# Performance work log

Measured on AMD Instinct MI355X. Metric: run time of the kernel, lower is better.

Reference implementation:

```python
import jax, jax.numpy as jnp
import numpy as np

NEG = -1e9  # finite stand-in for -inf (avoids inf-inf NaNs, safe in fp32)


def setup_inputs() -> dict:
    T, V, Lmax, A = 2048, 8192, 8, 64
    rng = np.random.default_rng(0)
    seq = rng.integers(0, A, size=T).astype(np.int32)
    # first A pieces are the single codepoints -> every sequence is segmentable
    piece_lens = np.concatenate([
        np.ones(A, np.int32),
        rng.integers(1, Lmax + 1, size=V - A).astype(np.int32),
    ])
    pieces = rng.integers(0, A, size=(V, Lmax)).astype(np.int32)
    pieces[:A, 0] = np.arange(A)
    logits = rng.standard_normal(V).astype(np.float32)
    m = logits.max()
    log_probs = (logits - m - np.log(np.exp(logits - m).sum())).astype(np.float32)
    return {
        'seq': jnp.asarray(seq),
        'pieces': jnp.asarray(pieces),
        'piece_lens': jnp.asarray(piece_lens),
        'log_probs': jnp.asarray(log_probs),
    }


def reference(seq, pieces, piece_lens, log_probs):
    T = seq.shape[0]
    V, Lmax = pieces.shape
    dt = log_probs.dtype

    # --- match table: match[t, i] = piece i matches sequence at position t ---
    seq_pad = jnp.concatenate([seq, jnp.full((Lmax,), -1, seq.dtype)])
    windows = seq_pad[jnp.arange(T)[:, None] + jnp.arange(Lmax)[None, :]]  # [T, Lmax]
    lmask = jnp.arange(Lmax)[None, :] < piece_lens[:, None]                # [V, Lmax]
    eq = windows[:, None, :] == pieces[None, :, :]                        # [T, V, Lmax]
    fits = (jnp.arange(T)[:, None] + piece_lens[None, :]) <= T            # [T, V]
    match = jnp.all(eq | ~lmask[None, :, :], axis=-1) & fits              # [T, V]
    mlp = jnp.where(match, log_probs[None, :], NEG).astype(dt)            # [T, V]

    # end_logp[t-1, i] = mlp[t - len_i, i]  (piece i ending exactly at t, t=1..T)
    te = jnp.arange(1, T + 1)[:, None]
    src = te - piece_lens[None, :]
    end_logp = jnp.where(src >= 0,
                         mlp[jnp.clip(src, 0, T - 1), jnp.arange(V)[None, :]],
                         NEG)

    # --- forward pass: alpha[t] = logsumexp_i alpha[t - len_i] + log p_i ---
    idx_a = Lmax - piece_lens  # window slot holding alpha[t - len_i]
    def fstep(win, row):
        a_t = jax.nn.logsumexp(win[idx_a] + row)
        return jnp.concatenate([win[1:], a_t[None]]), a_t
    win0 = jnp.full((Lmax,), NEG, dt).at[-1].set(0.0)
    _, alpha_rest = jax.lax.scan(fstep, win0, end_logp)
    alpha = jnp.concatenate([jnp.zeros((1,), dt), alpha_rest])  # [T+1]

    # --- backward pass: beta[t] = logsumexp_i log p_i + beta[t + len_i] ---
    idx_b = piece_lens - 1  # window slot holding beta[t + len_i]
    def bstep(win, row):
        b_t = jax.nn.logsumexp(row + win[idx_b])
        return jnp.concatenate([b_t[None], win[:-1]]), b_t
    winT = jnp.full((Lmax,), NEG, dt).at[0].set(0.0)
    _, beta_rev = jax.lax.scan(bstep, winT, mlp[::-1])
    beta = jnp.concatenate([beta_rev[::-1], jnp.zeros((1,), dt)])  # [T+1]

    # --- posteriors: P[t, i] = exp(alpha[t] + log p_i + beta[t+len_i] - alpha[T]) ---
    norm = alpha[T]
    beta_next = beta[jnp.clip(jnp.arange(T)[:, None] + piece_lens[None, :], 0, T)]
    P = jnp.exp(alpha[:T][:, None] + mlp + beta_next - norm)
    P = jnp.where(match, P, 0.0)
    return jnp.where(norm > NEG / 2, P, jnp.zeros_like(P))
```

## Files before the change

kernel.cpp:

```cpp
#include <hip/hip_runtime.h>
#include <stdint.h>

#define LMAX 8
#define KCH 32
#define NC  64
#define LN2D 0.6931471805599453

struct __align__(16) PK { unsigned long long key; float logp; int len; };

__device__ __forceinline__ int exp2i(double m) {
  return (int)((__double_as_longlong(m) >> 52) & 0x7ff) - 1023;
}
__device__ __forceinline__ double pow2d(int e) {
  return __longlong_as_double((long long)(1023 + e) << 52);
}

__global__ void k_prep(const int* __restrict__ seq, const int* __restrict__ pieces,
                       const int* __restrict__ plens, const float* __restrict__ logp,
                       PK* __restrict__ pk, unsigned long long* __restrict__ w64,
                       float* __restrict__ M, int T, int V) {
  int idx = blockIdx.x * blockDim.x + threadIdx.x;
  if (idx < V) {
    const int* pr = pieces + idx * LMAX;
    int len = plens[idx];
    unsigned long long key = 0ull;
    #pragma unroll
    for (int l = 0; l < LMAX; ++l) {
      unsigned long long b = (unsigned long long)(pr[l] & 0xFF);
      if (l < len) key |= b << (8 * l);
    }
    PK o; o.key = key; o.logp = logp[idx]; o.len = len;
    pk[idx] = o;
  } else if (idx < V + T) {
    int t = idx - V;
    unsigned long long w = 0ull;
    #pragma unroll
    for (int l = 0; l < LMAX; ++l) {
      int pos = t + l;
      unsigned long long b = (pos < T) ? (unsigned long long)(seq[pos] & 0xFF) : 0xFFull;
      w |= b << (8 * l);
    }
    w64[t] = w;
  } else if (idx < V + T + T * LMAX) {
    M[idx - V - T] = 0.f;
  }
}

__global__ void k_match(const PK* __restrict__ pk, const unsigned long long* __restrict__ w64,
                        float* __restrict__ M, int T, int V, int tPer) {
  int v = blockIdx.x * blockDim.x + threadIdx.x;
  PK p = pk[v];
  unsigned long long mask = (p.len >= 8) ? ~0ull : ((1ull << (8 * p.len)) - 1ull);
  unsigned long long key = p.key;
  int t0 = blockIdx.y * tPer;
  float prob = -1.f;
  for (int t = t0; t < t0 + tPer; ++t) {
    unsigned long long w = w64[t];
    if (((w ^ key) & mask) == 0ull) {
      if (prob < 0.f) prob = expf(p.logp);
      atomicAdd(&M[t * LMAX + (p.len - 1)], prob);
    }
  }
}

__global__ __launch_bounds__(256) void k_scan(const float* __restrict__ M,
        double* __restrict__ aD, double* __restrict__ bD,
        float* __restrict__ aL, float* __restrict__ bL, int T) {
  __shared__ float  Wt[2][64][65];
  __shared__ double Ust[2][NC][8];
  __shared__ int    EW[2][NC];
  __shared__ int    Eacc[2][NC];
  const int tid = threadIdx.x;
  const float4* Mv = (const float4*)M;

  {
    const int dir = tid >> 7;
    const int lt  = tid & 127;
    const int c   = lt >> 1, h = lt & 1;
    const int base = c * KCH;
    double st[8][4];
    #pragma unroll
    for (int i = 0; i < 8; ++i)
      #pragma unroll
      for (int bb = 0; bb < 4; ++bb)
        st[i][bb] = (i == 4 * h + bb) ? 1.0 : 0.0;

    if (dir == 0) {
      float4 ra = Mv[base * 2], rb = Mv[base * 2 + 1];
      for (int kg = 0; kg < KCH / 8; ++kg) {
        #pragma unroll
        for (int kk = 0; kk < 8; ++kk) {
          int k = kg * 8 + kk;
          float4 c0 = ra, c1 = rb;
          int nk = (k + 1 < KCH) ? k + 1 : KCH - 1;
          ra = Mv[(base + nk) * 2]; rb = Mv[(base + nk) * 2 + 1];
          double r0=c0.x,r1=c0.y,r2=c0.z,r3=c0.w,r4=c1.x,r5=c1.y,r6=c1.z,r7=c1.w;
          #pragma unroll
          for (int bb = 0; bb < 4; ++bb) {
            double a_ = st[kk & 7][bb];
            st[(kk+1)&7][bb] = fma(a_, r0, st[(kk+1)&7][bb]);
            st[(kk+2)&7][bb] = fma(a_, r1, st[(kk+2)&7][bb]);
            st[(kk+3)&7][bb] = fma(a_, r2, st[(kk+3)&7][bb]);
            st[(kk+4)&7][bb] = fma(a_, r3, st[(kk+4)&7][bb]);
            st[(kk+5)&7][bb] = fma(a_, r4, st[(kk+5)&7][bb]);
            st[(kk+6)&7][bb] = fma(a_, r5, st[(kk+6)&7][bb]);
            st[(kk+7)&7][bb] = fma(a_, r6, st[(kk+7)&7][bb]);
            st[kk & 7][bb]   = a_ * r7;
          }
        }
      }
    } else {
      float4 ra = Mv[(base + KCH - 1) * 2], rb = Mv[(base + KCH - 1) * 2 + 1];
      for (int kg = 0; kg < KCH / 8; ++kg) {
        #pragma unroll
        for (int kk = 0; kk < 8; ++kk) {
          int k = kg * 8 + kk;
          float4 c0 = ra, c1 = rb;
          int nk = (k + 1 < KCH) ? k + 1 : KCH - 1;
          int nt = base + KCH - 1 - nk;
          ra = Mv[nt * 2]; rb = Mv[nt * 2 + 1];
          double r0=c0.x,r1=c0.y,r2=c0.z,r3=c0.w,r4=c1.x,r5=c1.y,r6=c1.z,r7=c1.w;
          #pragma unroll
          for (int bb = 0; bb < 4; ++bb) {
            double nb =            r0 * st[(8 -kk)&7][bb];
            nb = fma(r1, st[(9 -kk)&7][bb], nb);
            nb = fma(r2, st[(10-kk)&7][bb], nb);
            nb = fma(r3, st[(11-kk)&7][bb], nb);
            nb = fma(r4, st[(12-kk)&7][bb], nb);
            nb = fma(r5, st[(13-kk)&7][bb], nb);
            nb = fma(r6, st[(14-kk)&7][bb], nb);
            nb = fma(r7, st[(15-kk)&7][bb], nb);
            st[(7 - kk) & 7][bb] = nb;
          }
        }
      }
    }
    double mx = 0.0;
    #pragma unroll
    for (int i = 0; i < 8; ++i)
      #pragma unroll
      for (int bb = 0; bb < 4; ++bb) mx = fmax(mx, st[i][bb]);
    mx = fmax(mx, __shfl_xor(mx, 1));
    int e = exp2i(mx);
    double sc = pow2d(-e);
    #pragma unroll
    for (int i = 0; i < 8; ++i)
      #pragma unroll
      for (int bb = 0; bb < 4; ++bb)
        Wt[dir][i * 8 + 4 * h + bb][c] = (float)(st[i][bb] * sc);
    if (h == 0) EW[dir][c] = e;
  }
  __syncthreads();

  {
    int wv = tid >> 6;
    if ((wv & 1) == 0) {
      const int dir = wv >> 1;
      const int l = tid & 63;
      double uj = ((l & 7) == 0) ? 1.0 : 0.0;
      int ea = 0;
      int c0 = dir ? (NC - 1) : 0;
      double wcur = (double)Wt[dir][l][c0];
      for (int ci = 0; ci < NC; ++ci) {
        int c = dir ? (NC - 1 - ci) : ci;
        int cn = dir ? (NC - 2 - ci) : (ci + 1);
        if (l < 8) Ust[dir][c][l] = uj;
        if (l == 0) Eacc[dir][c] = ea;
        double wnext = (ci + 1 < NC) ? (double)Wt[dir][l][cn] : 0.0;
        double p = wcur * uj;
        p += __shfl_xor(p, 1);
        p += __shfl_xor(p, 2);
        p += __shfl_xor(p, 4);
        uj = __shfl(p, ((l & 7) << 3) | (l >> 3));
        ea += EW[dir][c];
        if (ci & 1) {
          double m = uj;
          m = fmax(m, __shfl_xor(m, 1));
          m = fmax(m, __shfl_xor(m, 2));
          m = fmax(m, __shfl_xor(m, 4));
          int ex = exp2i(m);
          uj *= pow2d(-ex);
          ea += ex;
        }
        wcur = wnext;
      }
    }
  }
  __syncthreads();

  {
    int wv = tid >> 6;
    int c = tid & 63;
    int base = c * KCH;
    if (wv == 0) {
      double st[8];
      #pragma unroll
      for (int i = 0; i < 8; ++i) st[i] = Ust[0][c][i];
      float4 ra = Mv[base * 2], rb = Mv[base * 2 + 1];
      for (int kg = 0; kg < KCH / 8; ++kg) {
        #pragma unroll
        for (int kk = 0; kk < 8; ++kk) {
          int k = kg * 8 + kk;
          float4 c0 = ra, c1 = rb;
          int nk = (k + 1 < KCH) ? k + 1 : KCH - 1;
          ra = Mv[(base + nk) * 2]; rb = Mv[(base + nk) * 2 + 1];
          double r0=c0.x,r1=c0.y,r2=c0.z,r3=c0.w,r4=c1.x,r5=c1.y,r6=c1.z,r7=c1.w;
          double a_ = st[kk & 7];
          st[(kk+1)&7] = fma(a_, r0, st[(kk+1)&7]);
          st[(kk+2)&7] = fma(a_, r1, st[(kk+2)&7]);
          st[(kk+3)&7] = fma(a_, r2, st[(kk+3)&7]);
          st[(kk+4)&7] = fma(a_, r3, st[(kk+4)&7]);
          st[(kk+5)&7] = fma(a_, r4, st[(kk+5)&7]);
          st[(kk+6)&7] = fma(a_, r5, st[(kk+6)&7]);
          st[(kk+7)&7] = fma(a_, r6, st[(kk+7)&7]);
          st[kk & 7]   = a_ * r7;
          aD[base + k + 1] = st[(kk + 1) & 7];
        }
      }
    } else if (wv == 2) {
      double st[8];
      #pragma unroll
      for (int i = 0; i < 8; ++i) st[i] = Ust[1][c][i];
      float4 ra = Mv[(base + KCH - 1) * 2], rb = Mv[(base + KCH - 1) * 2 + 1];
      for (int kg = 0; kg < KCH / 8; ++kg) {
        #pragma unroll
        for (int kk = 0; kk < 8; ++kk) {
          int k = kg * 8 + kk;
          int t = base + KCH - 1 - k;
          float4 c0 = ra, c1 = rb;
          int nk = (k + 1 < KCH) ? k + 1 : KCH - 1;
          int nt = base + KCH - 1 - nk;
          ra = Mv[nt * 2]; rb = Mv[nt * 2 + 1];
          double r0=c0.x,r1=c0.y,r2=c0.z,r3=c0.w,r4=c1.x,r5=c1.y,r6=c1.z,r7=c1.w;
          double nb =            r0 * st[(8 -kk)&7];
          nb = fma(r1, st[(9 -kk)&7], nb);
          nb = fma(r2, st[(10-kk)&7], nb);
          nb = fma(r3, st[(11-kk)&7], nb);
          nb = fma(r4, st[(12-kk)&7], nb);
          nb = fma(r5, st[(13-kk)&7], nb);
          nb = fma(r6, st[(14-kk)&7], nb);
          nb = fma(r7, st[(15-kk)&7], nb);
          st[(7 - kk) & 7] = nb;
          bD[t] = nb;
        }
      }
    }
  }
  __syncthreads();

  for (int t = tid; t <= T; t += 256) {
    float av = 0.f, bv = 0.f;
    if (t > 0)  av = (float)(log(aD[t]) + (double)Eacc[0][(t - 1) >> 5] * LN2D);
    if (t < T)  bv = (float)(log(bD[t]) + (double)Eacc[1][t >> 5] * LN2D);
    aL[t] = av; bL[t] = bv;
  }
}

__global__ void k_out(const PK* __restrict__ pk, const unsigned long long* __restrict__ w64,
                      const float* __restrict__ aL, const float* __restrict__ bL,
                      float* __restrict__ out, int T, int V, int tPer) {
  int v = blockIdx.x * blockDim.x + threadIdx.x;
  PK p = pk[v];
  unsigned long long mask = (p.len >= 8) ? ~0ull : ((1ull << (8 * p.len)) - 1ull);
  unsigned long long key = p.key;
  float norm = aL[T];
  float base = p.logp - norm;
  int t0 = blockIdx.y * tPer;
  for (int t = t0; t < t0 + tPer; ++t) {
    unsigned long long w = w64[t];
    float val = 0.f;
    if (((w ^ key) & mask) == 0ull)
      val = __expf(aL[t] + base + bL[t + p.len]);
    out[(size_t)t * V + v] = val;
  }
}

extern "C" void kernel_launch(void* const* d_in, const int* in_sizes, int n_in,
                              void* d_out, int out_size, void* d_ws, size_t ws_size,
                              hipStream_t stream) {
  const int* seq    = (const int*)d_in[0];
  const int* pieces = (const int*)d_in[1];
  const int* plens  = (const int*)d_in[2];
  const float* logp = (const float*)d_in[3];
  float* out = (float*)d_out;
  const int T = in_sizes[0];
  const int V = in_sizes[2];

  char* p = (char*)d_ws;
  PK* pk = (PK*)p;                     p += (size_t)V * sizeof(PK);
  unsigned long long* w64 = (unsigned long long*)p; p += (size_t)T * 8;
  float* M = (float*)p;                p += (size_t)T * LMAX * 4;
  double* aD = (double*)p;             p += (size_t)(T + 1) * 8;
  double* bD = (double*)p;             p += (size_t)(T + 1) * 8;
  float* aL = (float*)p;               p += (size_t)(T + 1) * 4;
  float* bL = (float*)p;               p += (size_t)(T + 1) * 4;

  int prepN = V + T + T * LMAX;
  k_prep<<<(prepN + 255) / 256, 256, 0, stream>>>(seq, pieces, plens, logp, pk, w64, M, T, V);

  const int tPer2 = 128;
  dim3 g2(V / 256, T / tPer2);
  k_match<<<g2, 256, 0, stream>>>(pk, w64, M, T, V, tPer2);

  k_scan<<<1, 256, 0, stream>>>(M, aD, bD, aL, bL, T);

  const int tPer5 = 32;
  dim3 g5(V / 256, T / tPer5);
  k_out<<<g5, 256, 0, stream>>>(pk, w64, aL, bL, out, T, V, tPer5);
}
```

Measured before the change: 72.51 us.

## Replace serial chunk-carry scan with two-level parallel transfer-matrix scan in fp32

The single-block scan kernel now builds per-chunk 8x8 transfer matrices in fp32 with periodic power-of-two renormalisation, using 512 threads. The sequential 64-step carry propagation becomes a two-level scheme: eight groups compose eight chunks each, then a short serial scan over group products produces per-chunk prefix states. The log step also splits doubles into exponent and mantissa so it can use log2f instead of a double-precision log. The goal is to shorten the latency-bound serial chain in this one-block kernel, at the cost of more exponent bookkeeping, global scratch buffers for intermediate matrices, and extra synchronisation phases.

```diff
diff --git a/kernel.cpp b/kernel.cpp
--- a/kernel.cpp
+++ b/kernel.cpp
@@ -4,16 +4,16 @@
 #define LMAX 8
 #define KCH 32
 #define NC  64
+#define TT  2048
 #define LN2D 0.6931471805599453
+#define NEGE (-(1<<28))
 
 struct __align__(16) PK { unsigned long long key; float logp; int len; };
 
-__device__ __forceinline__ int exp2i(double m) {
-  return (int)((__double_as_longlong(m) >> 52) & 0x7ff) - 1023;
-}
-__device__ __forceinline__ double pow2d(int e) {
-  return __longlong_as_double((long long)(1023 + e) << 52);
-}
+__device__ __forceinline__ int fexp(float m) { return ((__float_as_int(m) >> 23) & 0xFF) - 127; }
+__device__ __forceinline__ int fexpbits(float m) { return (__float_as_int(m) >> 23) & 0xFF; }
+__device__ __forceinline__ float p2(int e) { return __int_as_float((e + 127) << 23); }
+__device__ __forceinline__ float p2c(int e) { return (e < -126) ? 0.f : p2(e); }
 
 __global__ void k_prep(const int* __restrict__ seq, const int* __restrict__ pieces,
                        const int* __restrict__ plens, const float* __restrict__ logp,
@@ -63,55 +63,73 @@
   }
 }
 
-__global__ __launch_bounds__(256) void k_scan(const float* __restrict__ M,
+__global__ __launch_bounds__(512) void k_scan(const float* __restrict__ M,
+        float* __restrict__ Wt, float* __restrict__ P,
         double* __restrict__ aD, double* __restrict__ bD,
-        float* __restrict__ aL, float* __restrict__ bL, int T) {
-  __shared__ float  Wt[2][64][65];
-  __shared__ double Ust[2][NC][8];
-  __shared__ int    EW[2][NC];
-  __shared__ int    Eacc[2][NC];
+        float* __restrict__ aL, float* __restrict__ bL) {
+  __shared__ float  Gm[2 * 8 * 69];
+  __shared__ float  Cs[2 * 64 * 9];
+  __shared__ float  Sg[2 * 8 * 9];
+  __shared__ int    EWc[2 * 64 * 8];
+  __shared__ int    EPs[2 * 64 * 8];
+  __shared__ int    EGs[2 * 8 * 8];
+  __shared__ int    EaccP[2 * 64];
+  __shared__ int    EsB[2 * 8];
   const int tid = threadIdx.x;
   const float4* Mv = (const float4*)M;
 
   {
-    const int dir = tid >> 7;
-    const int lt  = tid & 127;
-    const int c   = lt >> 1, h = lt & 1;
+    const int dir = tid >> 8, lt = tid & 255;
+    const int c = lt >> 2, h = lt & 3;
     const int base = c * KCH;
-    double st[8][4];
-    #pragma unroll
-    for (int i = 0; i < 8; ++i)
-      #pragma unroll
-      for (int bb = 0; bb < 4; ++bb)
-        st[i][bb] = (i == 4 * h + bb) ? 1.0 : 0.0;
-
+    float st[2][8];
+    #pragma unroll
+    for (int bb = 0; bb < 2; ++bb)
+      #pragma unroll
+      for (int i = 0; i < 8; ++i) st[bb][i] = (i == 2 * h + bb) ? p2(64) : 0.f;
+    int ec = -64;
     if (dir == 0) {
       float4 ra = Mv[base * 2], rb = Mv[base * 2 + 1];
-      for (int kg = 0; kg < KCH / 8; ++kg) {
+      for (int kg = 0; kg < 4; ++kg) {
         #pragma unroll
         for (int kk = 0; kk < 8; ++kk) {
           int k = kg * 8 + kk;
           float4 c0 = ra, c1 = rb;
           int nk = (k + 1 < KCH) ? k + 1 : KCH - 1;
           ra = Mv[(base + nk) * 2]; rb = Mv[(base + nk) * 2 + 1];
-          double r0=c0.x,r1=c0.y,r2=c0.z,r3=c0.w,r4=c1.x,r5=c1.y,r6=c1.z,r7=c1.w;
           #pragma unroll
-          for (int bb = 0; bb < 4; ++bb) {
-            double a_ = st[kk & 7][bb];
-            st[(kk+1)&7][bb] = fma(a_, r0, st[(kk+1)&7][bb]);
-            st[(kk+2)&7][bb] = fma(a_, r1, st[(kk+2)&7][bb]);
-            st[(kk+3)&7][bb] = fma(a_, r2, st[(kk+3)&7][bb]);
-            st[(kk+4)&7][bb] = fma(a_, r3, st[(kk+4)&7][bb]);
-            st[(kk+5)&7][bb] = fma(a_, r4, st[(kk+5)&7][bb]);
-            st[(kk+6)&7][bb] = fma(a_, r5, st[(kk+6)&7][bb]);
-            st[(kk+7)&7][bb] = fma(a_, r6, st[(kk+7)&7][bb]);
-            st[kk & 7][bb]   = a_ * r7;
+          for (int bb = 0; bb < 2; ++bb) {
+            float a_ = st[bb][kk & 7];
+            st[bb][(kk + 1) & 7] = fmaf(a_, c0.x, st[bb][(kk + 1) & 7]);
+            st[bb][(kk + 2) & 7] = fmaf(a_, c0.y, st[bb][(kk + 2) & 7]);
+            st[bb][(kk + 3) & 7] = fmaf(a_, c0.z, st[bb][(kk + 3) & 7]);
+            st[bb][(kk + 4) & 7] = fmaf(a_, c0.w, st[bb][(kk + 4) & 7]);
+            st[bb][(kk + 5) & 7] = fmaf(a_, c1.x, st[bb][(kk + 5) & 7]);
+            st[bb][(kk + 6) & 7] = fmaf(a_, c1.y, st[bb][(kk + 6) & 7]);
+            st[bb][(kk + 7) & 7] = fmaf(a_, c1.z, st[bb][(kk + 7) & 7]);
+            st[bb][kk & 7]       = a_ * c1.w;
+          }
+          if (kk == 3 || kk == 7) {
+            float mx = 0.f;
+            #pragma unroll
+            for (int bb = 0; bb < 2; ++bb)
+              #pragma unroll
+              for (int i = 0; i < 8; ++i) mx = fmaxf(mx, st[bb][i]);
+            if (fexpbits(mx) != 0) {
+              int e = fexp(mx), d = 64 - e;
+              float m1 = p2(d / 2), m2 = p2(d - d / 2);
+              #pragma unroll
+              for (int bb = 0; bb < 2; ++bb)
+                #pragma unroll
+                for (int i = 0; i < 8; ++i) st[bb][i] = st[bb][i] * m1 * m2;
+              ec += e - 64;
+            }
           }
         }
       }
     } else {
       float4 ra = Mv[(base + KCH - 1) * 2], rb = Mv[(base + KCH - 1) * 2 + 1];
-      for (int kg = 0; kg < KCH / 8; ++kg) {
+      for (int kg = 0; kg < 4; ++kg) {
         #pragma unroll
         for (int kk = 0; kk < 8; ++kk) {
           int k = kg * 8 + kk;
@@ -119,139 +137,275 @@
           int nk = (k + 1 < KCH) ? k + 1 : KCH - 1;
           int nt = base + KCH - 1 - nk;
           ra = Mv[nt * 2]; rb = Mv[nt * 2 + 1];
-          double r0=c0.x,r1=c0.y,r2=c0.z,r3=c0.w,r4=c1.x,r5=c1.y,r6=c1.z,r7=c1.w;
           #pragma unroll
-          for (int bb = 0; bb < 4; ++bb) {
-            double nb =            r0 * st[(8 -kk)&7][bb];
-            nb = fma(r1, st[(9 -kk)&7][bb], nb);
-            nb = fma(r2, st[(10-kk)&7][bb], nb);
-            nb = fma(r3, st[(11-kk)&7][bb], nb);
-            nb = fma(r4, st[(12-kk)&7][bb], nb);
-            nb = fma(r5, st[(13-kk)&7][bb], nb);
-            nb = fma(r6, st[(14-kk)&7][bb], nb);
-            nb = fma(r7, st[(15-kk)&7][bb], nb);
-            st[(7 - kk) & 7][bb] = nb;
+          for (int bb = 0; bb < 2; ++bb) {
+            float nb =      c0.x * st[bb][(8  - kk) & 7];
+            nb = fmaf(c0.y, st[bb][(9  - kk) & 7], nb);
+            nb = fmaf(c0.z, st[bb][(10 - kk) & 7], nb);
+            nb = fmaf(c0.w, st[bb][(11 - kk) & 7], nb);
+            nb = fmaf(c1.x, st[bb][(12 - kk) & 7], nb);
+            nb = fmaf(c1.y, st[bb][(13 - kk) & 7], nb);
+            nb = fmaf(c1.z, st[bb][(14 - kk) & 7], nb);
+            nb = fmaf(c1.w, st[bb][(15 - kk) & 7], nb);
+            st[bb][(7 - kk) & 7] = nb;
+          }
+          if (kk == 3 || kk == 7) {
+            float mx = 0.f;
+            #pragma unroll
+            for (int bb = 0; bb < 2; ++bb)
+              #pragma unroll
+              for (int i = 0; i < 8; ++i) mx = fmaxf(mx, st[bb][i]);
+            if (fexpbits(mx) != 0) {
+              int e = fexp(mx), d = 64 - e;
+              float m1 = p2(d / 2), m2 = p2(d - d / 2);
+              #pragma unroll
+              for (int bb = 0; bb < 2; ++bb)
+                #pragma unroll
+                for (int i = 0; i < 8; ++i) st[bb][i] = st[bb][i] * m1 * m2;
+              ec += e - 64;
+            }
           }
         }
       }
     }
-    double mx = 0.0;
-    #pragma unroll
-    for (int i = 0; i < 8; ++i)
-      #pragma unroll
-      for (int bb = 0; bb < 4; ++bb) mx = fmax(mx, st[i][bb]);
-    mx = fmax(mx, __shfl_xor(mx, 1));
-    int e = exp2i(mx);
-    double sc = pow2d(-e);
-    #pragma unroll
-    for (int i = 0; i < 8; ++i)
-      #pragma unroll
-      for (int bb = 0; bb < 4; ++bb)
-        Wt[dir][i * 8 + 4 * h + bb][c] = (float)(st[i][bb] * sc);
-    if (h == 0) EW[dir][c] = e;
+    float mx = 0.f;
+    #pragma unroll
+    for (int bb = 0; bb < 2; ++bb)
+      #pragma unroll
+      for (int i = 0; i < 8; ++i) mx = fmaxf(mx, st[bb][i]);
+    int lc = dir ? (NC - 1 - c) : c;
+    float* wp = Wt + (dir * 64 + lc) * 68;
+    int ew;
+    if (fexpbits(mx) == 0) {
+      ew = NEGE;
+      #pragma unroll
+      for (int bb = 0; bb < 2; ++bb)
+        #pragma unroll
+        for (int i = 0; i < 8; ++i) wp[(2 * h + bb) * 8 + i] = 0.f;
+    } else {
+      int e = fexp(mx);
+      float sc = p2(-e);
+      ew = ec + e;
+      #pragma unroll
+      for (int bb = 0; bb < 2; ++bb)
+        #pragma unroll
+        for (int i = 0; i < 8; ++i) wp[(2 * h + bb) * 8 + i] = st[bb][i] * sc;
+    }
+    EWc[(dir * 64 + lc) * 8 + 2 * h]     = ew;
+    EWc[(dir * 64 + lc) * 8 + 2 * h + 1] = ew;
   }
   __syncthreads();
 
-  {
-    int wv = tid >> 6;
-    if ((wv & 1) == 0) {
-      const int dir = wv >> 1;
-      const int l = tid & 63;
-      double uj = ((l & 7) == 0) ? 1.0 : 0.0;
-      int ea = 0;
-      int c0 = dir ? (NC - 1) : 0;
-      double wcur = (double)Wt[dir][l][c0];
-      for (int ci = 0; ci < NC; ++ci) {
-        int c = dir ? (NC - 1 - ci) : ci;
-        int cn = dir ? (NC - 2 - ci) : (ci + 1);
-        if (l < 8) Ust[dir][c][l] = uj;
-        if (l == 0) Eacc[dir][c] = ea;
-        double wnext = (ci + 1 < NC) ? (double)Wt[dir][l][cn] : 0.0;
-        double p = wcur * uj;
-        p += __shfl_xor(p, 1);
-        p += __shfl_xor(p, 2);
-        p += __shfl_xor(p, 4);
-        uj = __shfl(p, ((l & 7) << 3) | (l >> 3));
-        ea += EW[dir][c];
-        if (ci & 1) {
-          double m = uj;
-          m = fmax(m, __shfl_xor(m, 1));
-          m = fmax(m, __shfl_xor(m, 2));
-          m = fmax(m, __shfl_xor(m, 4));
-          int ex = exp2i(m);
-          uj *= pow2d(-ex);
-          ea += ex;
-        }
-        wcur = wnext;
-      }
-    }
+  if (tid < 128) {
+    const int dir = tid >> 6, w = (tid >> 3) & 7, b = tid & 7;
+    float v[8];
+    #pragma unroll
+    for (int i = 0; i < 8; ++i) v[i] = (i == b) ? 1.f : 0.f;
+    int ec = 0;
+    for (int c = 0; c < 8; ++c) {
+      int lc = w * 8 + c;
+      float* pp = P + (dir * 64 + lc) * 69 + b * 8;
+      #pragma unroll
+      for (int i = 0; i < 8; ++i) pp[i] = v[i];
+      EPs[(dir * 64 + lc) * 8 + b] = ec;
+      const float* wp = Wt + (dir * 64 + lc) * 68;
+      int ew[8];
+      #pragma unroll
+      for (int j = 0; j < 8; ++j) ew[j] = EWc[(dir * 64 + lc) * 8 + j];
+      int emax = ew[0];
+      #pragma unroll
+      for (int j = 1; j < 8; ++j) emax = max(emax, ew[j]);
+      float nv[8] = {0, 0, 0, 0, 0, 0, 0, 0};
+      #pragma unroll
+      for (int j = 0; j < 8; ++j) {
+        float tj = v[j] * p2c(ew[j] - emax + 64);
+        float4 ca = *(const float4*)(wp + j * 8);
+        float4 cb = *(const float4*)(wp + j * 8 + 4);
+        nv[0] = fmaf(tj, ca.x, nv[0]); nv[1] = fmaf(tj, ca.y, nv[1]);
+        nv[2] = fmaf(tj, ca.z, nv[2]); nv[3] = fmaf(tj, ca.w, nv[3]);
+        nv[4] = fmaf(tj, cb.x, nv[4]); nv[5] = fmaf(tj, cb.y, nv[5]);
+        nv[6] = fmaf(tj, cb.z, nv[6]); nv[7] = fmaf(tj, cb.w, nv[7]);
+      }
+      float mx = 0.f;
+      #pragma unroll
+      for (int i = 0; i < 8; ++i) mx = fmaxf(mx, nv[i]);
+      if (fexpbits(mx) == 0) {
+        #pragma unroll
+        for (int i = 0; i < 8; ++i) v[i] = 0.f;
+        ec = NEGE;
+      } else {
+        int e = fexp(mx);
+        float sc = p2(-e);
+        #pragma unroll
+        for (int i = 0; i < 8; ++i) v[i] = nv[i] * sc;
+        ec = ec + emax + e - 64;
+      }
+    }
+    float* gp = Gm + (dir * 8 + w) * 69 + b * 8;
+    #pragma unroll
+    for (int i = 0; i < 8; ++i) gp[i] = v[i];
+    EGs[(dir * 8 + w) * 8 + b] = ec;
   }
   __syncthreads();
 
-  {
-    int wv = tid >> 6;
-    int c = tid & 63;
-    int base = c * KCH;
-    if (wv == 0) {
-      double st[8];
-      #pragma unroll
-      for (int i = 0; i < 8; ++i) st[i] = Ust[0][c][i];
-      float4 ra = Mv[base * 2], rb = Mv[base * 2 + 1];
-      for (int kg = 0; kg < KCH / 8; ++kg) {
-        #pragma unroll
-        for (int kk = 0; kk < 8; ++kk) {
-          int k = kg * 8 + kk;
-          float4 c0 = ra, c1 = rb;
-          int nk = (k + 1 < KCH) ? k + 1 : KCH - 1;
-          ra = Mv[(base + nk) * 2]; rb = Mv[(base + nk) * 2 + 1];
-          double r0=c0.x,r1=c0.y,r2=c0.z,r3=c0.w,r4=c1.x,r5=c1.y,r6=c1.z,r7=c1.w;
-          double a_ = st[kk & 7];
-          st[(kk+1)&7] = fma(a_, r0, st[(kk+1)&7]);
-          st[(kk+2)&7] = fma(a_, r1, st[(kk+2)&7]);
-          st[(kk+3)&7] = fma(a_, r2, st[(kk+3)&7]);
-          st[(kk+4)&7] = fma(a_, r3, st[(kk+4)&7]);
-          st[(kk+5)&7] = fma(a_, r4, st[(kk+5)&7]);
-          st[(kk+6)&7] = fma(a_, r5, st[(kk+6)&7]);
-          st[(kk+7)&7] = fma(a_, r6, st[(kk+7)&7]);
-          st[kk & 7]   = a_ * r7;
-          aD[base + k + 1] = st[(kk + 1) & 7];
-        }
-      }
-    } else if (wv == 2) {
-      double st[8];
-      #pragma unroll
-      for (int i = 0; i < 8; ++i) st[i] = Ust[1][c][i];
-      float4 ra = Mv[(base + KCH - 1) * 2], rb = Mv[(base + KCH - 1) * 2 + 1];
-      for (int kg = 0; kg < KCH / 8; ++kg) {
-        #pragma unroll
-        for (int kk = 0; kk < 8; ++kk) {
-          int k = kg * 8 + kk;
-          int t = base + KCH - 1 - k;
-          float4 c0 = ra, c1 = rb;
-          int nk = (k + 1 < KCH) ? k + 1 : KCH - 1;
-          int nt = base + KCH - 1 - nk;
-          ra = Mv[nt * 2]; rb = Mv[nt * 2 + 1];
-          double r0=c0.x,r1=c0.y,r2=c0.z,r3=c0.w,r4=c1.x,r5=c1.y,r6=c1.z,r7=c1.w;
-          double nb =            r0 * st[(8 -kk)&7];
-          nb = fma(r1, st[(9 -kk)&7], nb);
-          nb = fma(r2, st[(10-kk)&7], nb);
-          nb = fma(r3, st[(11-kk)&7], nb);
-          nb = fma(r4, st[(12-kk)&7], nb);
-          nb = fma(r5, st[(13-kk)&7], nb);
-          nb = fma(r6, st[(14-kk)&7], nb);
-          nb = fma(r7, st[(15-kk)&7], nb);
-          st[(7 - kk) & 7] = nb;
-          bD[t] = nb;
-        }
-      }
+  if (tid < 8 || (tid >= 64 && tid < 72)) {
+    const int dir = (tid >= 64) ? 1 : 0, j = tid & 7;
+    float s[8];
+    #pragma unroll
+    for (int i = 0; i < 8; ++i) s[i] = (i == 0) ? 1.f : 0.f;
+    int Es = 0;
+    for (int w = 0; w < 8; ++w) {
+      float sj = s[0];
+      #pragma unroll
+      for (int i = 1; i < 8; ++i) if (j == i) sj = s[i];
+      Sg[(dir * 8 + w) * 9 + j] = sj;
+      if (j == 0) EsB[dir * 8 + w] = Es;
+      int eg[8];
+      #pragma unroll
+      for (int i = 0; i < 8; ++i) eg[i] = EGs[(dir * 8 + w) * 8 + i];
+      int egmax = eg[0];
+      #pragma unroll
+      for (int i = 1; i < 8; ++i) egmax = max(egmax, eg[i]);
+      int egj = eg[0];
+      #pragma unroll
+      for (int i = 1; i < 8; ++i) if (j == i) egj = eg[i];
+      float tb = sj * p2c(egj - egmax + 64);
+      const float* gp = Gm + (dir * 8 + w) * 69 + j * 8;
+      float p[8];
+      #pragma unroll
+      for (int i = 0; i < 8; ++i) p[i] = gp[i] * tb;
+      #pragma unroll
+      for (int m = 1; m <= 4; m <<= 1)
+        #pragma unroll
+        for (int i = 0; i < 8; ++i) p[i] += __shfl_xor(p[i], m);
+      float mx = 0.f;
+      #pragma unroll
+      for (int i = 0; i < 8; ++i) mx = fmaxf(mx, p[i]);
+      int e = fexp(mx);
+      float sc = p2(-e);
+      #pragma unroll
+      for (int i = 0; i < 8; ++i) s[i] = p[i] * sc;
+      Es += egmax + e - 64;
     }
   }
   __syncthreads();
 
-  for (int t = tid; t <= T; t += 256) {
+  if (tid < 128) {
+    const int dir = tid >> 6, lc = tid & 63, w = lc >> 3;
+    float sg[8];
+    #pragma unroll
+    for (int b = 0; b < 8; ++b) sg[b] = Sg[(dir * 8 + w) * 9 + b];
+    int Es = EsB[dir * 8 + w];
+    int ep[8];
+    #pragma unroll
+    for (int b = 0; b < 8; ++b) ep[b] = EPs[(dir * 64 + lc) * 8 + b];
+    int epmax = ep[0];
+    #pragma unroll
+    for (int b = 1; b < 8; ++b) epmax = max(epmax, ep[b]);
+    float cs[8] = {0, 0, 0, 0, 0, 0, 0, 0};
+    #pragma unroll
+    for (int b = 0; b < 8; ++b) {
+      float coef = sg[b] * p2c(ep[b] - epmax + 64);
+      const float* pp = P + (dir * 64 + lc) * 69 + b * 8;
+      #pragma unroll
+      for (int i = 0; i < 8; ++i) cs[i] = fmaf(coef, pp[i], cs[i]);
+    }
+    float mx = 0.f;
+    #pragma unroll
+    for (int i = 0; i < 8; ++i) mx = fmaxf(mx, cs[i]);
+    float* cp = Cs + (dir * 64 + lc) * 9;
+    int phys = dir ? (63 - lc) : lc;
+    if (fexpbits(mx) == 0) {
+      #pragma unroll
+      for (int i = 0; i < 8; ++i) cp[i] = 0.f;
+      EaccP[dir * 64 + phys] = NEGE;
+    } else {
+      int e = fexp(mx);
+      float sc = p2(-e);
+      #pragma unroll
+      for (int i = 0; i < 8; ++i) cp[i] = cs[i] * sc;
+      EaccP[dir * 64 + phys] = Es + epmax + e - 64;
+    }
+  }
+  __syncthreads();
+
+  if (tid < 64) {
+    int c = tid, base = c * KCH;
+    const float* cp = Cs + c * 9;
+    double st[8];
+    #pragma unroll
+    for (int i = 0; i < 8; ++i) st[i] = (double)cp[i];
+    float4 ra = Mv[base * 2], rb = Mv[base * 2 + 1];
+    for (int kg = 0; kg < KCH / 8; ++kg) {
+      #pragma unroll
+      for (int kk = 0; kk < 8; ++kk) {
+        int k = kg * 8 + kk;
+        float4 c0 = ra, c1 = rb;
+        int nk = (k + 1 < KCH) ? k + 1 : KCH - 1;
+        ra = Mv[(base + nk) * 2]; rb = Mv[(base + nk) * 2 + 1];
+        double r0 = c0.x, r1 = c0.y, r2 = c0.z, r3 = c0.w;
+        double r4 = c1.x, r5 = c1.y, r6 = c1.z, r7 = c1.w;
+        double a_ = st[kk & 7];
+        st[(kk + 1) & 7] = fma(a_, r0, st[(kk + 1) & 7]);
+        st[(kk + 2) & 7] = fma(a_, r1, st[(kk + 2) & 7]);
+        st[(kk + 3) & 7] = fma(a_, r2, st[(kk + 3) & 7]);
+        st[(kk + 4) & 7] = fma(a_, r3, st[(kk + 4) & 7]);
+        st[(kk + 5) & 7] = fma(a_, r4, st[(kk + 5) & 7]);
+        st[(kk + 6) & 7] = fma(a_, r5, st[(kk + 6) & 7]);
+        st[(kk + 7) & 7] = fma(a_, r6, st[(kk + 7) & 7]);
+        st[kk & 7]       = a_ * r7;
+        aD[base + k + 1] = st[(kk + 1) & 7];
+      }
+    }
+  } else if (tid < 128) {
+    int c = tid - 64, base = c * KCH;
+    const float* cp = Cs + (64 + 63 - c) * 9;
+    double st[8];
+    #pragma unroll
+    for (int i = 0; i < 8; ++i) st[i] = (double)cp[i];
+    float4 ra = Mv[(base + KCH - 1) * 2], rb = Mv[(base + KCH - 1) * 2 + 1];
+    for (int kg = 0; kg < KCH / 8; ++kg) {
+      #pragma unroll
+      for (int kk = 0; kk < 8; ++kk) {
+        int k = kg * 8 + kk;
+        int t = base + KCH - 1 - k;
+        float4 c0 = ra, c1 = rb;
+        int nk = (k + 1 < KCH) ? k + 1 : KCH - 1;
+        int nt = base + KCH - 1 - nk;
+        ra = Mv[nt * 2]; rb = Mv[nt * 2 + 1];
+        double r0 = c0.x, r1 = c0.y, r2 = c0.z, r3 = c0.w;
+        double r4 = c1.x, r5 = c1.y, r6 = c1.z, r7 = c1.w;
+        double nb =  r0 * st[(8  - kk) & 7];
+        nb = fma(r1, st[(9  - kk) & 7], nb);
+        nb = fma(r2, st[(10 - kk) & 7], nb);
+        nb = fma(r3, st[(11 - kk) & 7], nb);
+        nb = fma(r4, st[(12 - kk) & 7], nb);
+        nb = fma(r5, st[(13 - kk) & 7], nb);
+        nb = fma(r6, st[(14 - kk) & 7], nb);
+        nb = fma(r7, st[(15 - kk) & 7], nb);
+        st[(7 - kk) & 7] = nb;
+        bD[t] = nb;
+      }
+    }
+  }
+  __syncthreads();
+
+  for (int t = tid; t <= TT; t += 512) {
     float av = 0.f, bv = 0.f;
-    if (t > 0)  av = (float)(log(aD[t]) + (double)Eacc[0][(t - 1) >> 5] * LN2D);
-    if (t < T)  bv = (float)(log(bD[t]) + (double)Eacc[1][t >> 5] * LN2D);
+    if (t > 0) {
+      long long bits = __double_as_longlong(aD[t]);
+      int e2 = (int)((bits >> 52) & 0x7ff) - 1023;
+      double mant = __longlong_as_double((bits & 0xFFFFFFFFFFFFFLL) | 0x3FF0000000000000LL);
+      float lg = log2f((float)mant);
+      av = (float)(((double)(e2 + EaccP[(t - 1) >> 5]) + (double)lg) * LN2D);
+    }
+    if (t < TT) {
+      long long bits = __double_as_longlong(bD[t]);
+      int e2 = (int)((bits >> 52) & 0x7ff) - 1023;
+      double mant = __longlong_as_double((bits & 0xFFFFFFFFFFFFFLL) | 0x3FF0000000000000LL);
+      float lg = log2f((float)mant);
+      bv = (float)(((double)(e2 + EaccP[64 + (t >> 5)]) + (double)lg) * LN2D);
+    }
     aL[t] = av; bL[t] = bv;
   }
 }
@@ -287,13 +441,15 @@
   const int V = in_sizes[2];
 
   char* p = (char*)d_ws;
-  PK* pk = (PK*)p;                     p += (size_t)V * sizeof(PK);
-  unsigned long long* w64 = (unsigned long long*)p; p += (size_t)T * 8;
-  float* M = (float*)p;                p += (size_t)T * LMAX * 4;
-  double* aD = (double*)p;             p += (size_t)(T + 1) * 8;
-  double* bD = (double*)p;             p += (size_t)(T + 1) * 8;
-  float* aL = (float*)p;               p += (size_t)(T + 1) * 4;
-  float* bL = (float*)p;               p += (size_t)(T + 1) * 4;
+  PK* pk = (PK*)p;                                   p += (size_t)V * sizeof(PK);
+  unsigned long long* w64 = (unsigned long long*)p;  p += (size_t)T * 8;
+  float* M = (float*)p;                              p += (size_t)T * LMAX * 4;
+  double* aD = (double*)p;                           p += 16400;
+  double* bD = (double*)p;                           p += 16400;
+  float* aL = (float*)p;                             p += 8208;
+  float* bL = (float*)p;                             p += 8208;
+  float* Wt = (float*)p;                             p += (size_t)2 * 64 * 68 * 4;
+  float* Pm = (float*)p;                             p += (size_t)2 * 64 * 69 * 4;
 
   int prepN = V + T + T * LMAX;
   k_prep<<<(prepN + 255) / 256, 256, 0, stream>>>(seq, pieces, plens, logp, pk, w64, M, T, V);
@@ -302,7 +458,7 @@
   dim3 g2(V / 256, T / tPer2);
   k_match<<<g2, 256, 0, stream>>>(pk, w64, M, T, V, tPer2);
 
-  k_scan<<<1, 256, 0, stream>>>(M, aD, bD, aL, bL, T);
+  k_scan<<<1, 512, 0, stream>>>(M, Wt, Pm, aD, bD, aL, bL);
 
   const int tPer5 = 32;
   dim3 g5(V / 256, T / tPer5);
```

New measurement: 60.74 us. -16.2%, faster.
